# Kernel tuning notes

Measured on AMD Instinct MI355X. Metric: run time of the kernel, lower is better.

## Reference

```python
import jax, jax.numpy as jnp
import numpy as np

B, S, H, A = 64, 2048, 512, 512


def setup_inputs() -> dict:
    key = jax.random.key(0)
    k1, k2, k3, k4, k5 = jax.random.split(key, 5)
    nn_outs = jax.random.normal(k1, (B, S, H), dtype=jnp.float32)
    # lengths in [1, S] so every row has at least one valid step
    batch_lens = jax.random.randint(k2, (B,), 1, S + 1, dtype=jnp.int64)
    # learned params: context vector ~ U(-0.1, 0.1), Linear(H -> A)
    context = jax.random.uniform(k3, (A,), dtype=jnp.float32, minval=-0.1, maxval=0.1)
    proj_w = jax.random.uniform(k4, (A, H), dtype=jnp.float32, minval=-0.1, maxval=0.1)
    proj_b = jax.random.uniform(k5, (A,), dtype=jnp.float32, minval=-0.1, maxval=0.1)
    return {"nn_outs": nn_outs, "batch_lens": batch_lens,
            "context": context, "proj_w": proj_w, "proj_b": proj_b}


def reference(nn_outs, batch_lens, context, proj_w, proj_b):
    # proj = tanh(Linear(nn_outs)): (B, S, A)
    proj = jnp.tanh(jnp.einsum('bsh,ah->bsa', nn_outs, proj_w) + proj_b)
    # attention scores: (B, S)
    scores = jnp.einsum('bsa,a->bs', proj, context)
    # variable-length masked softmax (replaces the per-batch python loop)
    mask = jnp.arange(nn_outs.shape[1])[None, :] < batch_lens[:, None]  # (B, S)
    scores = jnp.where(mask, scores, -jnp.inf)
    atten = jax.nn.softmax(scores, axis=-1)
    atten = jnp.where(mask, atten, 0.0)  # padded positions exactly zero
    # weighted sum over steps: (B, H)
    return jnp.einsum('bs,bsh->bh', atten, nn_outs)
```

## Files before the change

### kernel.cpp

```cpp
#include <hip/hip_runtime.h>

#define BB 64
#define SS 2048
#define HH 512
#define MROWS (BB*SS)

typedef __attribute__((ext_vector_type(8))) short short8;
typedef __attribute__((ext_vector_type(4))) float f32x4;

__device__ inline unsigned short f2bf(float f){
  unsigned int u = __float_as_uint(f);
  u += 0x7FFFu + ((u >> 16) & 1u);
  return (unsigned short)(u >> 16);
}

__device__ inline int read_len(const void* lens, int i){
  const int* p = (const int*)lens;
  if (p[1] == 0) return (int)((const long long*)lens)[i];
  return p[i];
}

__device__ inline float fast_tanh(float x){
  x = fminf(fmaxf(x, -15.f), 15.f);
  float e = __expf(2.f * x);
  return (e - 1.f) / (e + 1.f);
}

__device__ inline void gload16(const void* gptr, void* lptr){
  __builtin_amdgcn_global_load_lds(
      (const __attribute__((address_space(1))) void*)gptr,
      (__attribute__((address_space(3))) void*)lptr, 16, 0, 0);
}

__device__ inline short8 cvt8p(float4 x0, float4 x1){
  short8 r;
  r[0] = (short)f2bf(x0.x); r[1] = (short)f2bf(x0.y);
  r[2] = (short)f2bf(x0.z); r[3] = (short)f2bf(x0.w);
  r[4] = (short)f2bf(x1.x); r[5] = (short)f2bf(x1.y);
  r[6] = (short)f2bf(x1.z); r[7] = (short)f2bf(x1.w);
  return r;
}

__global__ __launch_bounds__(256) void convw_kernel(
    const float* __restrict__ W, unsigned short* __restrict__ Wb)
{
  size_t base = (size_t)blockIdx.x * 64 * HH;
  int t = threadIdx.x;
  #pragma unroll
  for (int j = 0; j < 32; j++) {
    size_t idx = base + (size_t)j * 1024 + t * 4;
    float4 v = *(const float4*)(W + idx);
    unsigned int p0 = (unsigned int)f2bf(v.x) | ((unsigned int)f2bf(v.y) << 16);
    unsigned int p1 = (unsigned int)f2bf(v.z) | ((unsigned int)f2bf(v.w) << 16);
    *(uint2*)(Wb + idx) = make_uint2(p0, p1);
  }
}

__global__ __launch_bounds__(512, 2) void scores_n512(
    const float* __restrict__ X, const unsigned short* __restrict__ Wb,
    const void* __restrict__ lens, const float* __restrict__ ctx,
    const float* __restrict__ pb, float* __restrict__ scr)
{
  int bid = blockIdx.x;
  int mtile = (bid & 7) * 128 + (bid >> 3);
  int s_start = (mtile * 128) & (SS - 1);
  int b = (mtile * 128) >> 11;
  if (s_start >= read_len(lens, b)) return;

  __shared__ __align__(16) unsigned short As[128 * 64];
  __shared__ __align__(16) unsigned short Bs[2][512 * 64];

  int tid = threadIdx.x;
  int lane = tid & 63;
  int w = tid >> 6;
  int wm = w >> 2, wn = w & 3;
  int l15 = lane & 15, g = lane >> 4;

  f32x4 acc[4][8];
  #pragma unroll
  for (int i = 0; i < 4; i++)
    #pragma unroll
    for (int j = 0; j < 8; j++) acc[i][j] = (f32x4)0.f;

  int arow = tid >> 2;
  int alg0 = (tid & 3) * 2;
  const float* Ag = X + (size_t)(mtile * 128 + arow) * HH + alg0 * 8;
  int apg0 = (alg0)     ^ (arow & 7);
  int apg1 = (alg0 + 1) ^ (arow & 7);

  int brow = lane >> 3;
  int blg = (lane & 7) ^ brow;
  const unsigned short* Bg = Wb + (size_t)brow * HH + blg * 8;

  float4 ar[4];

#define A_ISSUE(KT) { const float* p_ = Ag + (KT); \
    ar[0] = *(const float4*)p_;       ar[1] = *(const float4*)(p_ + 4); \
    ar[2] = *(const float4*)(p_ + 8); ar[3] = *(const float4*)(p_ + 12); }

#define A_WRITE() { \
    *(short8*)&As[arow * 64 + apg0 * 8] = cvt8p(ar[0], ar[1]); \
    *(short8*)&As[arow * 64 + apg1 * 8] = cvt8p(ar[2], ar[3]); }

#define B_ISSUE(BUF, KT) { _Pragma("unroll") for (int i_ = 0; i_ < 8; i_++) { \
    int j_ = w * 8 + i_; \
    gload16(Bg + (size_t)(j_ * 8) * HH + (KT), &Bs[BUF][(j_ * 8) * 64]); } }

  A_ISSUE(0)
  B_ISSUE(0, 0)
  A_WRITE()
  __syncthreads();

  int cur = 0;
  for (int t = 0; t < 8; ++t) {
    if (t < 7) {
      A_ISSUE((t + 1) * 64)
      B_ISSUE(cur ^ 1, (t + 1) * 64)
    }
    #pragma unroll
    for (int kk = 0; kk < 64; kk += 32) {
      int ga = g + (kk >> 3);
      int pga = (ga ^ (l15 & 7)) * 8;
      short8 af[4];
      #pragma unroll
      for (int im = 0; im < 4; im++) {
        int r = wm * 64 + im * 16 + l15;
        af[im] = *(const short8*)&As[r * 64 + pga];
      }
      #pragma unroll
      for (int in = 0; in < 8; in++) {
        int r2 = wn * 128 + in * 16 + l15;
        short8 bfr = *(const short8*)&Bs[cur][r2 * 64 + pga];
        #pragma unroll
        for (int im = 0; im < 4; im++)
          acc[im][in] = __builtin_amdgcn_mfma_f32_16x16x32_bf16(
              af[im], bfr, acc[im][in], 0, 0, 0);
      }
    }
    __syncthreads();
    if (t < 7) A_WRITE()
    __syncthreads();
    cur ^= 1;
  }

  float pbv[8], ctxv[8];
  #pragma unroll
  for (int in = 0; in < 8; in++) {
    int a_g = wn * 128 + in * 16 + l15;
    pbv[in] = pb[a_g];
    ctxv[in] = ctx[a_g];
  }
  float* red = (float*)As;
  #pragma unroll
  for (int im = 0; im < 4; im++) {
    #pragma unroll
    for (int r = 0; r < 4; r++) {
      float rowsum = 0.f;
      #pragma unroll
      for (int in = 0; in < 8; in++)
        rowsum += fast_tanh(acc[im][in][r] + pbv[in]) * ctxv[in];
      #pragma unroll
      for (int m = 1; m < 16; m <<= 1)
        rowsum += __shfl_xor(rowsum, m, 64);
      if (l15 == 0)
        red[wn * 128 + wm * 64 + im * 16 + g * 4 + r] = rowsum;
    }
  }
  __syncthreads();
  if (tid < 128) {
    float s = red[tid] + red[128 + tid] + red[256 + tid] + red[384 + tid];
    scr[(size_t)mtile * 128 + tid] = s;
  }
}

__global__ __launch_bounds__(256) void softmax_kernel(
    const float* __restrict__ scr, const void* __restrict__ lens,
    float* __restrict__ wts)
{
  int b = blockIdx.x;
  int tid = threadIdx.x;
  int len = read_len(lens, b);
  float sc[8];
  #pragma unroll
  for (int i = 0; i < 8; i++)
    sc[i] = scr[(size_t)b * SS + tid + i * 256];
  float m = -1e30f;
  #pragma unroll
  for (int i = 0; i < 8; i++)
    if (tid + i * 256 < len) m = fmaxf(m, sc[i]);
  #pragma unroll
  for (int off = 1; off < 64; off <<= 1) m = fmaxf(m, __shfl_xor(m, off, 64));
  __shared__ float redm[4];
  __shared__ float reds[4];
  int w = tid >> 6, lane = tid & 63;
  if (lane == 0) redm[w] = m;
  __syncthreads();
  m = fmaxf(fmaxf(redm[0], redm[1]), fmaxf(redm[2], redm[3]));
  float e[8]; float sum = 0.f;
  #pragma unroll
  for (int i = 0; i < 8; i++) {
    int s = tid + i * 256;
    e[i] = (s < len) ? __expf(sc[i] - m) : 0.f;
    sum += e[i];
  }
  #pragma unroll
  for (int off = 1; off < 64; off <<= 1) sum += __shfl_xor(sum, off, 64);
  if (lane == 0) reds[w] = sum;
  __syncthreads();
  sum = reds[0] + reds[1] + reds[2] + reds[3];
  float inv = 1.f / sum;
  #pragma unroll
  for (int i = 0; i < 8; i++) {
    int s = tid + i * 256;
    wts[(size_t)b * SS + s] = e[i] * inv;
  }
}

__global__ __launch_bounds__(256) void softmax8_kernel(
    const float* __restrict__ sp, const void* __restrict__ lens,
    float* __restrict__ wts)
{
  int b = blockIdx.x;
  int tid = threadIdx.x;
  int len = read_len(lens, b);
  float sc[8];
  #pragma unroll
  for (int i = 0; i < 8; i++) {
    int s = tid + i * 256;
    size_t row = (size_t)b * SS + s;
    float v = 0.f;
    #pragma unroll
    for (int p = 0; p < 8; p++) v += sp[(size_t)p * MROWS + row];
    sc[i] = v;
  }
  float m = -1e30f;
  #pragma unroll
  for (int i = 0; i < 8; i++)
    if (tid + i * 256 < len) m = fmaxf(m, sc[i]);
  #pragma unroll
  for (int off = 1; off < 64; off <<= 1) m = fmaxf(m, __shfl_xor(m, off, 64));
  __shared__ float redm[4];
  __shared__ float reds[4];
  int w = tid >> 6, lane = tid & 63;
  if (lane == 0) redm[w] = m;
  __syncthreads();
  m = fmaxf(fmaxf(redm[0], redm[1]), fmaxf(redm[2], redm[3]));
  float e[8]; float sum = 0.f;
  #pragma unroll
  for (int i = 0; i < 8; i++) {
    int s = tid + i * 256;
    e[i] = (s < len) ? __expf(sc[i] - m) : 0.f;
    sum += e[i];
  }
  #pragma unroll
  for (int off = 1; off < 64; off <<= 1) sum += __shfl_xor(sum, off, 64);
  if (lane == 0) reds[w] = sum;
  __syncthreads();
  sum = reds[0] + reds[1] + reds[2] + reds[3];
  float inv = 1.f / sum;
  #pragma unroll
  for (int i = 0; i < 8; i++) {
    int s = tid + i * 256;
    wts[(size_t)b * SS + s] = e[i] * inv;
  }
}

__global__ __launch_bounds__(256) void wsum_kernel(
    const float* __restrict__ X, const float* __restrict__ wts,
    const void* __restrict__ lens, float* __restrict__ op)
{
  int sc = blockIdx.x;
  int b  = blockIdx.y;
  int tid = threadIdx.x;
  int s0 = sc * 128;
  int len = read_len(lens, b);
  int cnt = min(128, len - s0);
  float* o = op + ((size_t)sc * BB + b) * HH;
  if (cnt <= 0) {
    *(float2*)(o + tid * 2) = make_float2(0.f, 0.f);
    return;
  }
  __shared__ float wsh[128];
  __shared__ f32x4 red[128];
  if (tid < 128) wsh[tid] = wts[(size_t)b * SS + s0 + tid];
  __syncthreads();
  int h = (tid & 127) * 4;
  int sr = tid >> 7;
  f32x4 acc = (f32x4)0.f;
  for (int i = sr; i < cnt; i += 2) {
    float wv = wsh[i];
    const float* xr = X + ((size_t)b * SS + s0 + i) * HH + h;
    float4 xv = *(const float4*)xr;
    acc[0] += wv * xv.x;
    acc[1] += wv * xv.y;
    acc[2] += wv * xv.z;
    acc[3] += wv * xv.w;
  }
  if (sr == 1) red[tid & 127] = acc;
  __syncthreads();
  if (sr == 0) {
    f32x4 r2 = red[tid];
    acc[0] += r2[0]; acc[1] += r2[1]; acc[2] += r2[2]; acc[3] += r2[3];
    *(f32x4*)(o + h) = acc;
  }
}

__global__ __launch_bounds__(512) void reduce_kernel(
    const float* __restrict__ op, float* __restrict__ out)
{
  int b = blockIdx.x;
  int h = threadIdx.x;
  float v = 0.f;
  #pragma unroll
  for (int sc = 0; sc < 16; sc++) v += op[((size_t)sc * BB + b) * HH + h];
  out[(size_t)b * HH + h] = v;
}

__global__ __launch_bounds__(256) void scores_fb(
    const float* __restrict__ X, const void* __restrict__ lens,
    const float* __restrict__ ctx, const float* __restrict__ W,
    const float* __restrict__ pb, float* __restrict__ sp)
{
  int bid = blockIdx.x;
  int wg = (bid & 7) * 512 + (bid >> 3);
  int ntile = wg & 3;
  int mtile = wg >> 2;
  int s_start = (mtile * 128) & (SS - 1);
  int b = (mtile * 128) >> 11;
  if (s_start >= read_len(lens, b)) return;

  __shared__ unsigned short As[128 * 72];
  __shared__ unsigned short Bs[128 * 72];

  int tid = threadIdx.x;
  int lane = tid & 63;
  int w = tid >> 6;
  int wm = w >> 1, wn = w & 1;
  int l15 = lane & 15, g = lane >> 4;

  f32x4 acc[4][4];
  #pragma unroll
  for (int i = 0; i < 4; i++)
    #pragma unroll
    for (int j = 0; j < 4; j++) acc[i][j] = (f32x4)0.f;

  int srow = tid >> 4;
  int scol = (tid & 15) * 4;
  const float* Xbase = X + (size_t)(mtile * 128) * HH;
  const float* Wbase = W + (size_t)(ntile * 128) * HH;

  for (int kt = 0; kt < HH; kt += 64) {
    #pragma unroll
    for (int i = 0; i < 8; i++) {
      int row = srow + i * 16;
      float4 va = *(const float4*)(Xbase + (size_t)row * HH + kt + scol);
      unsigned int p0 = (unsigned int)f2bf(va.x) | ((unsigned int)f2bf(va.y) << 16);
      unsigned int p1 = (unsigned int)f2bf(va.z) | ((unsigned int)f2bf(va.w) << 16);
      *(uint2*)&As[row * 72 + scol] = make_uint2(p0, p1);
      float4 vb = *(const float4*)(Wbase + (size_t)row * HH + kt + scol);
      unsigned int q0 = (unsigned int)f2bf(vb.x) | ((unsigned int)f2bf(vb.y) << 16);
      unsigned int q1 = (unsigned int)f2bf(vb.z) | ((unsigned int)f2bf(vb.w) << 16);
      *(uint2*)&Bs[row * 72 + scol] = make_uint2(q0, q1);
    }
    __syncthreads();
    #pragma unroll
    for (int kk = 0; kk < 64; kk += 32) {
      short8 af[4], bfr[4];
      int ko = kk + g * 8;
      #pragma unroll
      for (int im = 0; im < 4; im++)
        af[im] = *(const short8*)&As[(wm * 64 + im * 16 + l15) * 72 + ko];
      #pragma unroll
      for (int in = 0; in < 4; in++)
        bfr[in] = *(const short8*)&Bs[(wn * 64 + in * 16 + l15) * 72 + ko];
      #pragma unroll
      for (int im = 0; im < 4; im++)
        #pragma unroll
        for (int in = 0; in < 4; in++)
          acc[im][in] = __builtin_amdgcn_mfma_f32_16x16x32_bf16(
              af[im], bfr[in], acc[im][in], 0, 0, 0);
    }
    __syncthreads();
  }

  #pragma unroll
  for (int im = 0; im < 4; im++) {
    #pragma unroll
    for (int r = 0; r < 4; r++) {
      float rowsum = 0.f;
      #pragma unroll
      for (int in = 0; in < 4; in++) {
        int a_g = ntile * 128 + wn * 64 + in * 16 + l15;
        rowsum += fast_tanh(acc[im][in][r] + pb[a_g]) * ctx[a_g];
      }
      #pragma unroll
      for (int m = 1; m < 16; m <<= 1)
        rowsum += __shfl_xor(rowsum, m, 64);
      if (l15 == 0) {
        int rowg = mtile * 128 + wm * 64 + im * 16 + g * 4 + r;
        sp[(size_t)(ntile * 2 + wn) * MROWS + rowg] = rowsum;
      }
    }
  }
}

extern "C" void kernel_launch(void* const* d_in, const int* in_sizes, int n_in,
                              void* d_out, int out_size, void* d_ws, size_t ws_size,
                              hipStream_t stream) {
  const float* X   = (const float*)d_in[0];
  const void*  lens = d_in[1];
  const float* ctx = (const float*)d_in[2];
  const float* W   = (const float*)d_in[3];
  const float* pb  = (const float*)d_in[4];
  float* out = (float*)d_out;

  char* ws = (char*)d_ws;
  const size_t WB_BYTES = (size_t)HH * HH * 2;
  const size_t SC_BYTES = (size_t)MROWS * 4;
  const size_t WT_BYTES = (size_t)BB * SS * 4;
  const size_t OP_BYTES = 16ull * BB * HH * 4;
  const size_t NEED = WB_BYTES + SC_BYTES + WT_BYTES + OP_BYTES;

  if (ws_size >= NEED) {
    unsigned short* Wb = (unsigned short*)ws;
    float* scr = (float*)(ws + WB_BYTES);
    float* wts = (float*)(ws + WB_BYTES + SC_BYTES);
    float* op  = (float*)(ws + WB_BYTES + SC_BYTES + WT_BYTES);

    convw_kernel<<<8, 256, 0, stream>>>(W, Wb);
    scores_n512<<<1024, 512, 0, stream>>>(X, Wb, lens, ctx, pb, scr);
    softmax_kernel<<<BB, 256, 0, stream>>>(scr, lens, wts);
    wsum_kernel<<<dim3(16, BB), 256, 0, stream>>>(X, wts, lens, op);
    reduce_kernel<<<BB, 512, 0, stream>>>(op, out);
  } else {
    const size_t SP_BYTES = 8ull * MROWS * 4;
    float* sp  = (float*)ws;
    float* wts = (float*)(ws + SP_BYTES);
    float* op  = (float*)(ws + SP_BYTES + WT_BYTES);

    scores_fb<<<4096, 256, 0, stream>>>(X, lens, ctx, W, pb, sp);
    softmax8_kernel<<<BB, 256, 0, stream>>>(sp, lens, wts);
    wsum_kernel<<<dim3(16, BB), 256, 0, stream>>>(X, wts, lens, op);
    reduce_kernel<<<BB, 512, 0, stream>>>(op, out);
  }
}
```

Baseline: 131.4 us.

## Fuse softmax and weighted sum into scores kernel with flash-style partial combine

```diff
diff --git a/kernel.cpp b/kernel.cpp
--- a/kernel.cpp
+++ b/kernel.cpp
@@ -56,16 +56,18 @@
   }
 }
 
-__global__ __launch_bounds__(512, 2) void scores_n512(
+__global__ __launch_bounds__(512, 2) void scores_fused(
     const float* __restrict__ X, const unsigned short* __restrict__ Wb,
     const void* __restrict__ lens, const float* __restrict__ ctx,
-    const float* __restrict__ pb, float* __restrict__ scr)
-{
-  int bid = blockIdx.x;
-  int mtile = (bid & 7) * 128 + (bid >> 3);
+    const float* __restrict__ pb, float* __restrict__ P,
+    float* __restrict__ pm, float* __restrict__ ps)
+{
+  int mtile = blockIdx.x;
   int s_start = (mtile * 128) & (SS - 1);
   int b = (mtile * 128) >> 11;
-  if (s_start >= read_len(lens, b)) return;
+  int len = read_len(lens, b);
+  if (s_start >= len) return;
+  int cnt = min(128, len - s_start);
 
   __shared__ __align__(16) unsigned short As[128 * 64];
   __shared__ __align__(16) unsigned short Bs[2][512 * 64];
@@ -109,14 +111,19 @@
   A_ISSUE(0)
   B_ISSUE(0, 0)
   A_WRITE()
-  __syncthreads();
+  asm volatile("s_waitcnt lgkmcnt(0)" ::: "memory");
+  __builtin_amdgcn_s_barrier();
 
   int cur = 0;
   for (int t = 0; t < 8; ++t) {
     if (t < 7) {
       A_ISSUE((t + 1) * 64)
       B_ISSUE(cur ^ 1, (t + 1) * 64)
-    }
+      asm volatile("s_waitcnt vmcnt(12)" ::: "memory");
+    } else {
+      asm volatile("s_waitcnt vmcnt(0)" ::: "memory");
+    }
+    __builtin_amdgcn_sched_barrier(0);
     #pragma unroll
     for (int kk = 0; kk < 64; kk += 32) {
       int ga = g + (kk >> 3);
@@ -137,9 +144,12 @@
               af[im], bfr, acc[im][in], 0, 0, 0);
       }
     }
-    __syncthreads();
-    if (t < 7) A_WRITE()
-    __syncthreads();
+    __builtin_amdgcn_s_barrier();
+    if (t < 7) {
+      A_WRITE()
+      asm volatile("s_waitcnt lgkmcnt(0)" ::: "memory");
+    }
+    __builtin_amdgcn_s_barrier();
     cur ^= 1;
   }
 
@@ -150,7 +160,10 @@
     pbv[in] = pb[a_g];
     ctxv[in] = ctx[a_g];
   }
-  float* red = (float*)As;
+  float* red  = (float*)As;
+  float* wsh  = ((float*)As) + 512;
+  float* wrd  = ((float*)As) + 640;
+  float* wrd2 = ((float*)As) + 644;
   #pragma unroll
   for (int im = 0; im < 4; im++) {
     #pragma unroll
@@ -167,153 +180,55 @@
     }
   }
   __syncthreads();
+  float sc = 0.f;
+  if (tid < 128)
+    sc = red[tid] + red[128 + tid] + red[256 + tid] + red[384 + tid];
+  float v = (tid < 128 && tid < cnt) ? sc : -1e30f;
+  #pragma unroll
+  for (int off = 1; off < 64; off <<= 1) v = fmaxf(v, __shfl_xor(v, off, 64));
+  if (tid < 128 && (tid & 63) == 0) wrd[tid >> 6] = v;
+  __syncthreads();
+  float m_loc = fmaxf(wrd[0], wrd[1]);
+  float e = 0.f;
   if (tid < 128) {
-    float s = red[tid] + red[128 + tid] + red[256 + tid] + red[384 + tid];
-    scr[(size_t)mtile * 128 + tid] = s;
-  }
-}
-
-__global__ __launch_bounds__(256) void softmax_kernel(
-    const float* __restrict__ scr, const void* __restrict__ lens,
-    float* __restrict__ wts)
+    e = (tid < cnt) ? __expf(sc - m_loc) : 0.f;
+    wsh[tid] = e;
+  }
+  float s1 = e;
+  #pragma unroll
+  for (int off = 1; off < 64; off <<= 1) s1 += __shfl_xor(s1, off, 64);
+  if (tid < 128 && (tid & 63) == 0) wrd2[tid >> 6] = s1;
+  __syncthreads();
+  if (tid == 0) {
+    pm[mtile] = m_loc;
+    ps[mtile] = wrd2[0] + wrd2[1];
+  }
+  const float* Xr = X + (size_t)(mtile * 128) * HH + tid;
+  float accp = 0.f;
+  #pragma unroll 4
+  for (int i = 0; i < cnt; ++i)
+    accp += wsh[i] * Xr[(size_t)i * HH];
+  P[(size_t)mtile * HH + tid] = accp;
+}
+
+__global__ __launch_bounds__(512) void combine_kernel(
+    const float* __restrict__ P, const float* __restrict__ pm,
+    const float* __restrict__ ps, const void* __restrict__ lens,
+    float* __restrict__ out)
 {
   int b = blockIdx.x;
   int tid = threadIdx.x;
   int len = read_len(lens, b);
-  float sc[8];
-  #pragma unroll
-  for (int i = 0; i < 8; i++)
-    sc[i] = scr[(size_t)b * SS + tid + i * 256];
+  int nblk = (len + 127) >> 7;
   float m = -1e30f;
-  #pragma unroll
-  for (int i = 0; i < 8; i++)
-    if (tid + i * 256 < len) m = fmaxf(m, sc[i]);
-  #pragma unroll
-  for (int off = 1; off < 64; off <<= 1) m = fmaxf(m, __shfl_xor(m, off, 64));
-  __shared__ float redm[4];
-  __shared__ float reds[4];
-  int w = tid >> 6, lane = tid & 63;
-  if (lane == 0) redm[w] = m;
-  __syncthreads();
-  m = fmaxf(fmaxf(redm[0], redm[1]), fmaxf(redm[2], redm[3]));
-  float e[8]; float sum = 0.f;
-  #pragma unroll
-  for (int i = 0; i < 8; i++) {
-    int s = tid + i * 256;
-    e[i] = (s < len) ? __expf(sc[i] - m) : 0.f;
-    sum += e[i];
-  }
-  #pragma unroll
-  for (int off = 1; off < 64; off <<= 1) sum += __shfl_xor(sum, off, 64);
-  if (lane == 0) reds[w] = sum;
-  __syncthreads();
-  sum = reds[0] + reds[1] + reds[2] + reds[3];
-  float inv = 1.f / sum;
-  #pragma unroll
-  for (int i = 0; i < 8; i++) {
-    int s = tid + i * 256;
-    wts[(size_t)b * SS + s] = e[i] * inv;
-  }
-}
-
-__global__ __launch_bounds__(256) void softmax8_kernel(
-    const float* __restrict__ sp, const void* __restrict__ lens,
-    float* __restrict__ wts)
-{
-  int b = blockIdx.x;
-  int tid = threadIdx.x;
-  int len = read_len(lens, b);
-  float sc[8];
-  #pragma unroll
-  for (int i = 0; i < 8; i++) {
-    int s = tid + i * 256;
-    size_t row = (size_t)b * SS + s;
-    float v = 0.f;
-    #pragma unroll
-    for (int p = 0; p < 8; p++) v += sp[(size_t)p * MROWS + row];
-    sc[i] = v;
-  }
-  float m = -1e30f;
-  #pragma unroll
-  for (int i = 0; i < 8; i++)
-    if (tid + i * 256 < len) m = fmaxf(m, sc[i]);
-  #pragma unroll
-  for (int off = 1; off < 64; off <<= 1) m = fmaxf(m, __shfl_xor(m, off, 64));
-  __shared__ float redm[4];
-  __shared__ float reds[4];
-  int w = tid >> 6, lane = tid & 63;
-  if (lane == 0) redm[w] = m;
-  __syncthreads();
-  m = fmaxf(fmaxf(redm[0], redm[1]), fmaxf(redm[2], redm[3]));
-  float e[8]; float sum = 0.f;
-  #pragma unroll
-  for (int i = 0; i < 8; i++) {
-    int s = tid + i * 256;
-    e[i] = (s < len) ? __expf(sc[i] - m) : 0.f;
-    sum += e[i];
-  }
-  #pragma unroll
-  for (int off = 1; off < 64; off <<= 1) sum += __shfl_xor(sum, off, 64);
-  if (lane == 0) reds[w] = sum;
-  __syncthreads();
-  sum = reds[0] + reds[1] + reds[2] + reds[3];
-  float inv = 1.f / sum;
-  #pragma unroll
-  for (int i = 0; i < 8; i++) {
-    int s = tid + i * 256;
-    wts[(size_t)b * SS + s] = e[i] * inv;
-  }
-}
-
-__global__ __launch_bounds__(256) void wsum_kernel(
-    const float* __restrict__ X, const float* __restrict__ wts,
-    const void* __restrict__ lens, float* __restrict__ op)
-{
-  int sc = blockIdx.x;
-  int b  = blockIdx.y;
-  int tid = threadIdx.x;
-  int s0 = sc * 128;
-  int len = read_len(lens, b);
-  int cnt = min(128, len - s0);
-  float* o = op + ((size_t)sc * BB + b) * HH;
-  if (cnt <= 0) {
-    *(float2*)(o + tid * 2) = make_float2(0.f, 0.f);
-    return;
-  }
-  __shared__ float wsh[128];
-  __shared__ f32x4 red[128];
-  if (tid < 128) wsh[tid] = wts[(size_t)b * SS + s0 + tid];
-  __syncthreads();
-  int h = (tid & 127) * 4;
-  int sr = tid >> 7;
-  f32x4 acc = (f32x4)0.f;
-  for (int i = sr; i < cnt; i += 2) {
-    float wv = wsh[i];
-    const float* xr = X + ((size_t)b * SS + s0 + i) * HH + h;
-    float4 xv = *(const float4*)xr;
-    acc[0] += wv * xv.x;
-    acc[1] += wv * xv.y;
-    acc[2] += wv * xv.z;
-    acc[3] += wv * xv.w;
-  }
-  if (sr == 1) red[tid & 127] = acc;
-  __syncthreads();
-  if (sr == 0) {
-    f32x4 r2 = red[tid];
-    acc[0] += r2[0]; acc[1] += r2[1]; acc[2] += r2[2]; acc[3] += r2[3];
-    *(f32x4*)(o + h) = acc;
-  }
-}
-
-__global__ __launch_bounds__(512) void reduce_kernel(
-    const float* __restrict__ op, float* __restrict__ out)
-{
-  int b = blockIdx.x;
-  int h = threadIdx.x;
-  float v = 0.f;
-  #pragma unroll
-  for (int sc = 0; sc < 16; sc++) v += op[((size_t)sc * BB + b) * HH + h];
-  out[(size_t)b * HH + h] = v;
+  for (int k = 0; k < nblk; ++k) m = fmaxf(m, pm[b * 16 + k]);
+  float S = 0.f, acc = 0.f;
+  for (int k = 0; k < nblk; ++k) {
+    float f = __expf(pm[b * 16 + k] - m);
+    S += f * ps[b * 16 + k];
+    acc += f * P[(size_t)(b * 16 + k) * HH + tid];
+  }
+  out[(size_t)b * HH + tid] = acc / S;
 }
 
 __global__ __launch_bounds__(256) void scores_fb(
@@ -404,6 +319,89 @@
   }
 }
 
+__global__ __launch_bounds__(256) void softmax8_kernel(
+    const float* __restrict__ sp, const void* __restrict__ lens,
+    float* __restrict__ wts)
+{
+  int b = blockIdx.x;
+  int tid = threadIdx.x;
+  int len = read_len(lens, b);
+  float sc[8];
+  #pragma unroll
+  for (int i = 0; i < 8; i++) {
+    int s = tid + i * 256;
+    size_t row = (size_t)b * SS + s;
+    float v = 0.f;
+    #pragma unroll
+    for (int p = 0; p < 8; p++) v += sp[(size_t)p * MROWS + row];
+    sc[i] = v;
+  }
+  float m = -1e30f;
+  #pragma unroll
+  for (int i = 0; i < 8; i++)
+    if (tid + i * 256 < len) m = fmaxf(m, sc[i]);
+  #pragma unroll
+  for (int off = 1; off < 64; off <<= 1) m = fmaxf(m, __shfl_xor(m, off, 64));
+  __shared__ float redm[4];
+  __shared__ float reds[4];
+  int w = tid >> 6, lane = tid & 63;
+  if (lane == 0) redm[w] = m;
+  __syncthreads();
+  m = fmaxf(fmaxf(redm[0], redm[1]), fmaxf(redm[2], redm[3]));
+  float e[8]; float sum = 0.f;
+  #pragma unroll
+  for (int i = 0; i < 8; i++) {
+    int s = tid + i * 256;
+    e[i] = (s < len) ? __expf(sc[i] - m) : 0.f;
+    sum += e[i];
+  }
+  #pragma unroll
+  for (int off = 1; off < 64; off <<= 1) sum += __shfl_xor(sum, off, 64);
+  if (lane == 0) reds[w] = sum;
+  __syncthreads();
+  sum = reds[0] + reds[1] + reds[2] + reds[3];
+  float inv = 1.f / sum;
+  #pragma unroll
+  for (int i = 0; i < 8; i++) {
+    int s = tid + i * 256;
+    wts[(size_t)b * SS + s] = e[i] * inv;
+  }
+}
+
+__global__ __launch_bounds__(256) void wsum_fb(
+    const float* __restrict__ X, const float* __restrict__ wts,
+    float* __restrict__ op)
+{
+  int sc = blockIdx.x;
+  int b  = blockIdx.y;
+  int tid = threadIdx.x;
+  float a0 = 0.f, a1 = 0.f;
+  int s0 = sc * 128;
+  for (int i = 0; i < 128; i++) {
+    int s = s0 + i;
+    float wv = wts[(size_t)b * SS + s];
+    if (wv != 0.f) {
+      const float* xr = X + ((size_t)b * SS + s) * HH;
+      a0 += wv * xr[tid];
+      a1 += wv * xr[tid + 256];
+    }
+  }
+  float* o = op + ((size_t)sc * BB + b) * HH;
+  o[tid] = a0;
+  o[tid + 256] = a1;
+}
+
+__global__ __launch_bounds__(512) void reduce_kernel(
+    const float* __restrict__ op, float* __restrict__ out)
+{
+  int b = blockIdx.x;
+  int h = threadIdx.x;
+  float v = 0.f;
+  #pragma unroll
+  for (int sc = 0; sc < 16; sc++) v += op[((size_t)sc * BB + b) * HH + h];
+  out[(size_t)b * HH + h] = v;
+}
+
 extern "C" void kernel_launch(void* const* d_in, const int* in_sizes, int n_in,
                               void* d_out, int out_size, void* d_ws, size_t ws_size,
                               hipStream_t stream) {
@@ -416,31 +414,29 @@
 
   char* ws = (char*)d_ws;
   const size_t WB_BYTES = (size_t)HH * HH * 2;
-  const size_t SC_BYTES = (size_t)MROWS * 4;
-  const size_t WT_BYTES = (size_t)BB * SS * 4;
-  const size_t OP_BYTES = 16ull * BB * HH * 4;
-  const size_t NEED = WB_BYTES + SC_BYTES + WT_BYTES + OP_BYTES;
+  const size_t P_BYTES  = 1024ull * HH * 4;
+  const size_t PM_BYTES = 1024 * 4;
+  const size_t NEED = WB_BYTES + P_BYTES + 2 * PM_BYTES;
 
   if (ws_size >= NEED) {
     unsigned short* Wb = (unsigned short*)ws;
-    float* scr = (float*)(ws + WB_BYTES);
-    float* wts = (float*)(ws + WB_BYTES + SC_BYTES);
-    float* op  = (float*)(ws + WB_BYTES + SC_BYTES + WT_BYTES);
+    float* P  = (float*)(ws + WB_BYTES);
+    float* pm = (float*)(ws + WB_BYTES + P_BYTES);
+    float* ps = (float*)(ws + WB_BYTES + P_BYTES + PM_BYTES);
 
     convw_kernel<<<8, 256, 0, stream>>>(W, Wb);
-    scores_n512<<<1024, 512, 0, stream>>>(X, Wb, lens, ctx, pb, scr);
-    softmax_kernel<<<BB, 256, 0, stream>>>(scr, lens, wts);
-    wsum_kernel<<<dim3(16, BB), 256, 0, stream>>>(X, wts, lens, op);
-    reduce_kernel<<<BB, 512, 0, stream>>>(op, out);
+    scores_fused<<<1024, 512, 0, stream>>>(X, Wb, lens, ctx, pb, P, pm, ps);
+    combine_kernel<<<BB, 512, 0, stream>>>(P, pm, ps, lens, out);
   } else {
     const size_t SP_BYTES = 8ull * MROWS * 4;
+    const size_t WT_BYTES = (size_t)BB * SS * 4;
     float* sp  = (float*)ws;
     float* wts = (float*)(ws + SP_BYTES);
     float* op  = (float*)(ws + SP_BYTES + WT_BYTES);
 
     scores_fb<<<4096, 256, 0, stream>>>(X, lens, ctx, W, pb, sp);
     softmax8_kernel<<<BB, 256, 0, stream>>>(sp, lens, wts);
-    wsum_kernel<<<dim3(16, BB), 256, 0, stream>>>(X, wts, lens, op);
+    wsum_fb<<<dim3(16, BB), 256, 0, stream>>>(X, wts, op);
     reduce_kernel<<<BB, 512, 0, stream>>>(op, out);
   }
 }
```

Result: slower. 182.6 us (+38.9%).

## Fuse softmax, weighted sum and reduction; widen scores GEMM to 1024 threads

Applied to the files above, without the earlier changes.

```diff
diff --git a/kernel.cpp b/kernel.cpp
--- a/kernel.cpp
+++ b/kernel.cpp
@@ -56,13 +56,12 @@
   }
 }
 
-__global__ __launch_bounds__(512, 2) void scores_n512(
+__global__ __launch_bounds__(1024) void scores_n512(
     const float* __restrict__ X, const unsigned short* __restrict__ Wb,
     const void* __restrict__ lens, const float* __restrict__ ctx,
     const float* __restrict__ pb, float* __restrict__ scr)
 {
-  int bid = blockIdx.x;
-  int mtile = (bid & 7) * 128 + (bid >> 3);
+  int mtile = blockIdx.x;
   int s_start = (mtile * 128) & (SS - 1);
   int b = (mtile * 128) >> 11;
   if (s_start >= read_len(lens, b)) return;
@@ -73,38 +72,34 @@
   int tid = threadIdx.x;
   int lane = tid & 63;
   int w = tid >> 6;
-  int wm = w >> 2, wn = w & 3;
+  int wm = w >> 3, wn = w & 7;
   int l15 = lane & 15, g = lane >> 4;
 
-  f32x4 acc[4][8];
+  f32x4 acc[4][4];
   #pragma unroll
   for (int i = 0; i < 4; i++)
     #pragma unroll
-    for (int j = 0; j < 8; j++) acc[i][j] = (f32x4)0.f;
-
-  int arow = tid >> 2;
-  int alg0 = (tid & 3) * 2;
-  const float* Ag = X + (size_t)(mtile * 128 + arow) * HH + alg0 * 8;
-  int apg0 = (alg0)     ^ (arow & 7);
-  int apg1 = (alg0 + 1) ^ (arow & 7);
-
-  int brow = lane >> 3;
-  int blg = (lane & 7) ^ brow;
-  const unsigned short* Bg = Wb + (size_t)brow * HH + blg * 8;
-
-  float4 ar[4];
+    for (int j = 0; j < 4; j++) acc[i][j] = (f32x4)0.f;
+
+  int arow = tid >> 3;
+  int alg  = tid & 7;
+  const float* Ag = X + (size_t)(mtile * 128 + arow) * HH + alg * 8;
+  int apg = alg ^ (arow & 7);
+
+  int blrow = lane >> 3;
+  int blg = (lane & 7) ^ blrow;
+  const unsigned short* Bg = Wb + (size_t)(w * 32 + blrow) * HH + blg * 8;
+
+  float4 ar0, ar1;
 
 #define A_ISSUE(KT) { const float* p_ = Ag + (KT); \
-    ar[0] = *(const float4*)p_;       ar[1] = *(const float4*)(p_ + 4); \
-    ar[2] = *(const float4*)(p_ + 8); ar[3] = *(const float4*)(p_ + 12); }
-
-#define A_WRITE() { \
-    *(short8*)&As[arow * 64 + apg0 * 8] = cvt8p(ar[0], ar[1]); \
-    *(short8*)&As[arow * 64 + apg1 * 8] = cvt8p(ar[2], ar[3]); }
-
-#define B_ISSUE(BUF, KT) { _Pragma("unroll") for (int i_ = 0; i_ < 8; i_++) { \
-    int j_ = w * 8 + i_; \
-    gload16(Bg + (size_t)(j_ * 8) * HH + (KT), &Bs[BUF][(j_ * 8) * 64]); } }
+    ar0 = *(const float4*)p_; ar1 = *(const float4*)(p_ + 4); }
+
+#define A_WRITE() { *(short8*)&As[arow * 64 + apg * 8] = cvt8p(ar0, ar1); }
+
+#define B_ISSUE(BUF, KT) { _Pragma("unroll") for (int i_ = 0; i_ < 4; i_++) { \
+    gload16(Bg + (size_t)(i_ * 8) * HH + (KT), \
+            &Bs[BUF][(w * 32 + i_ * 8) * 64]); } }
 
   A_ISSUE(0)
   B_ISSUE(0, 0)
@@ -128,8 +123,8 @@
         af[im] = *(const short8*)&As[r * 64 + pga];
       }
       #pragma unroll
-      for (int in = 0; in < 8; in++) {
-        int r2 = wn * 128 + in * 16 + l15;
+      for (int in = 0; in < 4; in++) {
+        int r2 = wn * 64 + in * 16 + l15;
         short8 bfr = *(const short8*)&Bs[cur][r2 * 64 + pga];
         #pragma unroll
         for (int im = 0; im < 4; im++)
@@ -143,10 +138,10 @@
     cur ^= 1;
   }
 
-  float pbv[8], ctxv[8];
-  #pragma unroll
-  for (int in = 0; in < 8; in++) {
-    int a_g = wn * 128 + in * 16 + l15;
+  float pbv[4], ctxv[4];
+  #pragma unroll
+  for (int in = 0; in < 4; in++) {
+    int a_g = wn * 64 + in * 16 + l15;
     pbv[in] = pb[a_g];
     ctxv[in] = ctx[a_g];
   }
@@ -157,24 +152,179 @@
     for (int r = 0; r < 4; r++) {
       float rowsum = 0.f;
       #pragma unroll
-      for (int in = 0; in < 8; in++)
+      for (int in = 0; in < 4; in++)
         rowsum += fast_tanh(acc[im][in][r] + pbv[in]) * ctxv[in];
       #pragma unroll
       for (int m = 1; m < 16; m <<= 1)
         rowsum += __shfl_xor(rowsum, m, 64);
-      if (l15 == 0)
-        red[wn * 128 + wm * 64 + im * 16 + g * 4 + r] = rowsum;
+      if (l15 == 0) {
+        int rowg = wm * 64 + im * 16 + g * 4 + r;
+        red[wn * 128 + rowg] = rowsum;
+      }
     }
   }
   __syncthreads();
   if (tid < 128) {
-    float s = red[tid] + red[128 + tid] + red[256 + tid] + red[384 + tid];
+    float s = 0.f;
+    #pragma unroll
+    for (int q = 0; q < 8; q++) s += red[q * 128 + tid];
     scr[(size_t)mtile * 128 + tid] = s;
   }
 }
 
-__global__ __launch_bounds__(256) void softmax_kernel(
-    const float* __restrict__ scr, const void* __restrict__ lens,
+__global__ __launch_bounds__(256) void finish_kernel(
+    const float* __restrict__ X, const float* __restrict__ scr,
+    const void* __restrict__ lens, float* __restrict__ out)
+{
+  int qa = blockIdx.x;
+  int b  = blockIdx.y;
+  int tid = threadIdx.x;
+  int lane = tid & 63;
+  int wv = tid >> 6;
+  int len = read_len(lens, b);
+
+  __shared__ float esh[SS];
+  __shared__ float redm_[4], reds_[4];
+  __shared__ float red2[256];
+
+  float sc[8];
+  float m = -1e30f;
+  #pragma unroll
+  for (int i = 0; i < 8; i++) {
+    int s = tid + i * 256;
+    sc[i] = scr[(size_t)b * SS + s];
+    if (s < len) m = fmaxf(m, sc[i]);
+  }
+  #pragma unroll
+  for (int off = 1; off < 64; off <<= 1) m = fmaxf(m, __shfl_xor(m, off, 64));
+  if (lane == 0) redm_[wv] = m;
+  __syncthreads();
+  m = fmaxf(fmaxf(redm_[0], redm_[1]), fmaxf(redm_[2], redm_[3]));
+
+  float sum = 0.f;
+  #pragma unroll
+  for (int i = 0; i < 8; i++) {
+    int s = tid + i * 256;
+    float e = (s < len) ? __expf(sc[i] - m) : 0.f;
+    esh[s] = e;
+    sum += e;
+  }
+  #pragma unroll
+  for (int off = 1; off < 64; off <<= 1) sum += __shfl_xor(sum, off, 64);
+  if (lane == 0) reds_[wv] = sum;
+  __syncthreads();
+  float inv = 1.f / (reds_[0] + reds_[1] + reds_[2] + reds_[3]);
+
+  int h = qa * 64 + lane;
+  int sr = wv;
+  const float* Xc = X + (size_t)b * SS * HH + h;
+  float a0 = 0.f, a1 = 0.f, a2 = 0.f, a3 = 0.f;
+  int i = sr;
+  for (; i + 12 < len; i += 16) {
+    a0 += esh[i]      * Xc[(size_t)(i)      * HH];
+    a1 += esh[i + 4]  * Xc[(size_t)(i + 4)  * HH];
+    a2 += esh[i + 8]  * Xc[(size_t)(i + 8)  * HH];
+    a3 += esh[i + 12] * Xc[(size_t)(i + 12) * HH];
+  }
+  for (; i < len; i += 4)
+    a0 += esh[i] * Xc[(size_t)i * HH];
+  red2[tid] = (a0 + a1) + (a2 + a3);
+  __syncthreads();
+  if (sr == 0)
+    out[(size_t)b * HH + h] =
+        (red2[tid] + red2[tid + 64] + red2[tid + 128] + red2[tid + 192]) * inv;
+}
+
+__global__ __launch_bounds__(256) void scores_fb(
+    const float* __restrict__ X, const void* __restrict__ lens,
+    const float* __restrict__ ctx, const float* __restrict__ W,
+    const float* __restrict__ pb, float* __restrict__ sp)
+{
+  int bid = blockIdx.x;
+  int wg = (bid & 7) * 512 + (bid >> 3);
+  int ntile = wg & 3;
+  int mtile = wg >> 2;
+  int s_start = (mtile * 128) & (SS - 1);
+  int b = (mtile * 128) >> 11;
+  if (s_start >= read_len(lens, b)) return;
+
+  __shared__ unsigned short As[128 * 72];
+  __shared__ unsigned short Bs[128 * 72];
+
+  int tid = threadIdx.x;
+  int lane = tid & 63;
+  int w = tid >> 6;
+  int wm = w >> 1, wn = w & 1;
+  int l15 = lane & 15, g = lane >> 4;
+
+  f32x4 acc[4][4];
+  #pragma unroll
+  for (int i = 0; i < 4; i++)
+    #pragma unroll
+    for (int j = 0; j < 4; j++) acc[i][j] = (f32x4)0.f;
+
+  int srow = tid >> 4;
+  int scol = (tid & 15) * 4;
+  const float* Xbase = X + (size_t)(mtile * 128) * HH;
+  const float* Wbase = W + (size_t)(ntile * 128) * HH;
+
+  for (int kt = 0; kt < HH; kt += 64) {
+    #pragma unroll
+    for (int i = 0; i < 8; i++) {
+      int row = srow + i * 16;
+      float4 va = *(const float4*)(Xbase + (size_t)row * HH + kt + scol);
+      unsigned int p0 = (unsigned int)f2bf(va.x) | ((unsigned int)f2bf(va.y) << 16);
+      unsigned int p1 = (unsigned int)f2bf(va.z) | ((unsigned int)f2bf(va.w) << 16);
+      *(uint2*)&As[row * 72 + scol] = make_uint2(p0, p1);
+      float4 vb = *(const float4*)(Wbase + (size_t)row * HH + kt + scol);
+      unsigned int q0 = (unsigned int)f2bf(vb.x) | ((unsigned int)f2bf(vb.y) << 16);
+      unsigned int q1 = (unsigned int)f2bf(vb.z) | ((unsigned int)f2bf(vb.w) << 16);
+      *(uint2*)&Bs[row * 72 + scol] = make_uint2(q0, q1);
+    }
+    __syncthreads();
+    #pragma unroll
+    for (int kk = 0; kk < 64; kk += 32) {
+      short8 af[4], bfr[4];
+      int ko = kk + g * 8;
+      #pragma unroll
+      for (int im = 0; im < 4; im++)
+        af[im] = *(const short8*)&As[(wm * 64 + im * 16 + l15) * 72 + ko];
+      #pragma unroll
+      for (int in = 0; in < 4; in++)
+        bfr[in] = *(const short8*)&Bs[(wn * 64 + in * 16 + l15) * 72 + ko];
+      #pragma unroll
+      for (int im = 0; im < 4; im++)
+        #pragma unroll
+        for (int in = 0; in < 4; in++)
+          acc[im][in] = __builtin_amdgcn_mfma_f32_16x16x32_bf16(
+              af[im], bfr[in], acc[im][in], 0, 0, 0);
+    }
+    __syncthreads();
+  }
+
+  #pragma unroll
+  for (int im = 0; im < 4; im++) {
+    #pragma unroll
+    for (int r = 0; r < 4; r++) {
+      float rowsum = 0.f;
+      #pragma unroll
+      for (int in = 0; in < 4; in++) {
+        int a_g = ntile * 128 + wn * 64 + in * 16 + l15;
+        rowsum += fast_tanh(acc[im][in][r] + pb[a_g]) * ctx[a_g];
+      }
+      #pragma unroll
+      for (int m = 1; m < 16; m <<= 1)
+        rowsum += __shfl_xor(rowsum, m, 64);
+      if (l15 == 0) {
+        int rowg = mtile * 128 + wm * 64 + im * 16 + g * 4 + r;
+        sp[(size_t)(ntile * 2 + wn) * MROWS + rowg] = rowsum;
+      }
+    }
+  }
+}
+
+__global__ __launch_bounds__(256) void softmax8_kernel(
+    const float* __restrict__ sp, const void* __restrict__ lens,
     float* __restrict__ wts)
 {
   int b = blockIdx.x;
@@ -182,8 +332,14 @@
   int len = read_len(lens, b);
   float sc[8];
   #pragma unroll
-  for (int i = 0; i < 8; i++)
-    sc[i] = scr[(size_t)b * SS + tid + i * 256];
+  for (int i = 0; i < 8; i++) {
+    int s = tid + i * 256;
+    size_t row = (size_t)b * SS + s;
+    float v = 0.f;
+    #pragma unroll
+    for (int p = 0; p < 8; p++) v += sp[(size_t)p * MROWS + row];
+    sc[i] = v;
+  }
   float m = -1e30f;
   #pragma unroll
   for (int i = 0; i < 8; i++)
@@ -216,56 +372,7 @@
   }
 }
 
-__global__ __launch_bounds__(256) void softmax8_kernel(
-    const float* __restrict__ sp, const void* __restrict__ lens,
-    float* __restrict__ wts)
-{
-  int b = blockIdx.x;
-  int tid = threadIdx.x;
-  int len = read_len(lens, b);
-  float sc[8];
-  #pragma unroll
-  for (int i = 0; i < 8; i++) {
-    int s = tid + i * 256;
-    size_t row = (size_t)b * SS + s;
-    float v = 0.f;
-    #pragma unroll
-    for (int p = 0; p < 8; p++) v += sp[(size_t)p * MROWS + row];
-    sc[i] = v;
-  }
-  float m = -1e30f;
-  #pragma unroll
-  for (int i = 0; i < 8; i++)
-    if (tid + i * 256 < len) m = fmaxf(m, sc[i]);
-  #pragma unroll
-  for (int off = 1; off < 64; off <<= 1) m = fmaxf(m, __shfl_xor(m, off, 64));
-  __shared__ float redm[4];
-  __shared__ float reds[4];
-  int w = tid >> 6, lane = tid & 63;
-  if (lane == 0) redm[w] = m;
-  __syncthreads();
-  m = fmaxf(fmaxf(redm[0], redm[1]), fmaxf(redm[2], redm[3]));
-  float e[8]; float sum = 0.f;
-  #pragma unroll
-  for (int i = 0; i < 8; i++) {
-    int s = tid + i * 256;
-    e[i] = (s < len) ? __expf(sc[i] - m) : 0.f;
-    sum += e[i];
-  }
-  #pragma unroll
-  for (int off = 1; off < 64; off <<= 1) sum += __shfl_xor(sum, off, 64);
-  if (lane == 0) reds[w] = sum;
-  __syncthreads();
-  sum = reds[0] + reds[1] + reds[2] + reds[3];
-  float inv = 1.f / sum;
-  #pragma unroll
-  for (int i = 0; i < 8; i++) {
-    int s = tid + i * 256;
-    wts[(size_t)b * SS + s] = e[i] * inv;
-  }
-}
-
-__global__ __launch_bounds__(256) void wsum_kernel(
+__global__ __launch_bounds__(256) void wsum_fb(
     const float* __restrict__ X, const float* __restrict__ wts,
     const void* __restrict__ lens, float* __restrict__ op)
 {
@@ -316,94 +423,6 @@
   out[(size_t)b * HH + h] = v;
 }
 
-__global__ __launch_bounds__(256) void scores_fb(
-    const float* __restrict__ X, const void* __restrict__ lens,
-    const float* __restrict__ ctx, const float* __restrict__ W,
-    const float* __restrict__ pb, float* __restrict__ sp)
-{
-  int bid = blockIdx.x;
-  int wg = (bid & 7) * 512 + (bid >> 3);
-  int ntile = wg & 3;
-  int mtile = wg >> 2;
-  int s_start = (mtile * 128) & (SS - 1);
-  int b = (mtile * 128) >> 11;
-  if (s_start >= read_len(lens, b)) return;
-
-  __shared__ unsigned short As[128 * 72];
-  __shared__ unsigned short Bs[128 * 72];
-
-  int tid = threadIdx.x;
-  int lane = tid & 63;
-  int w = tid >> 6;
-  int wm = w >> 1, wn = w & 1;
-  int l15 = lane & 15, g = lane >> 4;
-
-  f32x4 acc[4][4];
-  #pragma unroll
-  for (int i = 0; i < 4; i++)
-    #pragma unroll
-    for (int j = 0; j < 4; j++) acc[i][j] = (f32x4)0.f;
-
-  int srow = tid >> 4;
-  int scol = (tid & 15) * 4;
-  const float* Xbase = X + (size_t)(mtile * 128) * HH;
-  const float* Wbase = W + (size_t)(ntile * 128) * HH;
-
-  for (int kt = 0; kt < HH; kt += 64) {
-    #pragma unroll
-    for (int i = 0; i < 8; i++) {
-      int row = srow + i * 16;
-      float4 va = *(const float4*)(Xbase + (size_t)row * HH + kt + scol);
-      unsigned int p0 = (unsigned int)f2bf(va.x) | ((unsigned int)f2bf(va.y) << 16);
-      unsigned int p1 = (unsigned int)f2bf(va.z) | ((unsigned int)f2bf(va.w) << 16);
-      *(uint2*)&As[row * 72 + scol] = make_uint2(p0, p1);
-      float4 vb = *(const float4*)(Wbase + (size_t)row * HH + kt + scol);
-      unsigned int q0 = (unsigned int)f2bf(vb.x) | ((unsigned int)f2bf(vb.y) << 16);
-      unsigned int q1 = (unsigned int)f2bf(vb.z) | ((unsigned int)f2bf(vb.w) << 16);
-      *(uint2*)&Bs[row * 72 + scol] = make_uint2(q0, q1);
-    }
-    __syncthreads();
-    #pragma unroll
-    for (int kk = 0; kk < 64; kk += 32) {
-      short8 af[4], bfr[4];
-      int ko = kk + g * 8;
-      #pragma unroll
-      for (int im = 0; im < 4; im++)
-        af[im] = *(const short8*)&As[(wm * 64 + im * 16 + l15) * 72 + ko];
-      #pragma unroll
-      for (int in = 0; in < 4; in++)
-        bfr[in] = *(const short8*)&Bs[(wn * 64 + in * 16 + l15) * 72 + ko];
-      #pragma unroll
-      for (int im = 0; im < 4; im++)
-        #pragma unroll
-        for (int in = 0; in < 4; in++)
-          acc[im][in] = __builtin_amdgcn_mfma_f32_16x16x32_bf16(
-              af[im], bfr[in], acc[im][in], 0, 0, 0);
-    }
-    __syncthreads();
-  }
-
-  #pragma unroll
-  for (int im = 0; im < 4; im++) {
-    #pragma unroll
-    for (int r = 0; r < 4; r++) {
-      float rowsum = 0.f;
-      #pragma unroll
-      for (int in = 0; in < 4; in++) {
-        int a_g = ntile * 128 + wn * 64 + in * 16 + l15;
-        rowsum += fast_tanh(acc[im][in][r] + pb[a_g]) * ctx[a_g];
-      }
-      #pragma unroll
-      for (int m = 1; m < 16; m <<= 1)
-        rowsum += __shfl_xor(rowsum, m, 64);
-      if (l15 == 0) {
-        int rowg = mtile * 128 + wm * 64 + im * 16 + g * 4 + r;
-        sp[(size_t)(ntile * 2 + wn) * MROWS + rowg] = rowsum;
-      }
-    }
-  }
-}
-
 extern "C" void kernel_launch(void* const* d_in, const int* in_sizes, int n_in,
                               void* d_out, int out_size, void* d_ws, size_t ws_size,
                               hipStream_t stream) {
@@ -417,30 +436,25 @@
   char* ws = (char*)d_ws;
   const size_t WB_BYTES = (size_t)HH * HH * 2;
   const size_t SC_BYTES = (size_t)MROWS * 4;
-  const size_t WT_BYTES = (size_t)BB * SS * 4;
-  const size_t OP_BYTES = 16ull * BB * HH * 4;
-  const size_t NEED = WB_BYTES + SC_BYTES + WT_BYTES + OP_BYTES;
+  const size_t NEED = WB_BYTES + SC_BYTES;
 
   if (ws_size >= NEED) {
     unsigned short* Wb = (unsigned short*)ws;
     float* scr = (float*)(ws + WB_BYTES);
-    float* wts = (float*)(ws + WB_BYTES + SC_BYTES);
-    float* op  = (float*)(ws + WB_BYTES + SC_BYTES + WT_BYTES);
 
     convw_kernel<<<8, 256, 0, stream>>>(W, Wb);
-    scores_n512<<<1024, 512, 0, stream>>>(X, Wb, lens, ctx, pb, scr);
-    softmax_kernel<<<BB, 256, 0, stream>>>(scr, lens, wts);
-    wsum_kernel<<<dim3(16, BB), 256, 0, stream>>>(X, wts, lens, op);
-    reduce_kernel<<<BB, 512, 0, stream>>>(op, out);
+    scores_n512<<<1024, 1024, 0, stream>>>(X, Wb, lens, ctx, pb, scr);
+    finish_kernel<<<dim3(8, BB), 256, 0, stream>>>(X, scr, lens, out);
   } else {
     const size_t SP_BYTES = 8ull * MROWS * 4;
+    const size_t WT_BYTES = (size_t)BB * SS * 4;
     float* sp  = (float*)ws;
     float* wts = (float*)(ws + SP_BYTES);
     float* op  = (float*)(ws + SP_BYTES + WT_BYTES);
 
     scores_fb<<<4096, 256, 0, stream>>>(X, lens, ctx, W, pb, sp);
     softmax8_kernel<<<BB, 256, 0, stream>>>(sp, lens, wts);
-    wsum_kernel<<<dim3(16, BB), 256, 0, stream>>>(X, wts, lens, op);
+    wsum_fb<<<dim3(16, BB), 256, 0, stream>>>(X, wts, lens, op);
     reduce_kernel<<<BB, 512, 0, stream>>>(op, out);
   }
 }
```

Result: slower. 165.8 us (+26.1%).
